# Kernel optimization log

Hardware: AMD Instinct MI355X
Metric: run time of the kernel (lower is better)

## Reference

```python
import math
import jax, jax.numpy as jnp
import numpy as np

NUM_HEADS = 16
LN_EPS = 1e-5


def _ln(x, g, b):
    m = x.mean(-1, keepdims=True)
    v = ((x - m) ** 2).mean(-1, keepdims=True)
    return (x - m) * jax.lax.rsqrt(v + LN_EPS) * g + b


def _rotary_embedding(lat, lon, dim, base=10000.0):
    # spherical-geometry-aware rotary phases; returns sin/cos of shape lat.shape + [dim//2]
    pi = jnp.asarray(math.pi, lat.dtype)
    lon_wrapped = jnp.remainder(lon + pi, 2 * pi) - pi
    lat_c = jnp.clip(lat, -math.pi / 2 + 1e-6, math.pi / 2 - 1e-6)
    scaled_lon = lon_wrapped * jnp.cos(lat_c)
    half = dim // 2
    inv_freq = 1.0 / (base ** (jnp.arange(half, dtype=lat.dtype) / half))
    phase = (lat_c + scaled_lon)[..., None] * inv_freq
    return jnp.sin(phase), jnp.cos(phase)


def _apply_rotary(q, k, sin, cos):
    # q,k: [N, heads, S, hd]; sin/cos: [S, hd//2]
    sin = sin[None, None]
    cos = cos[None, None]
    def rot(x):
        x1 = x[..., 0::2]  # even lanes (torch view(...,hd//2,2).unbind(-1))
        x2 = x[..., 1::2]
        # torch concatenates the two rotated halves (no re-interleave)
        return jnp.concatenate([x1 * cos - x2 * sin, x1 * sin + x2 * cos], axis=-1)
    return rot(q), rot(k)


def _sdpa(q, k, v):
    scale = 1.0 / jnp.sqrt(jnp.asarray(q.shape[-1], q.dtype))
    s = jnp.einsum('nhqd,nhkd->nhqk', q, k) * scale
    return jnp.einsum('nhqk,nhkd->nhqd', jax.nn.softmax(s, axis=-1), v)


def _axial_block(tokens, g, bln, qkv_w, qkv_b, proj_w, proj_b, sincos):
    # tokens: [N, S, D] -> norm -> qkv -> (rope) -> sdpa -> proj -> residual
    N, S, D = tokens.shape
    hd = D // NUM_HEADS
    qkv = _ln(tokens, g, bln) @ qkv_w + qkv_b
    q, k, v = jnp.split(qkv, 3, axis=-1)
    def to_heads(t):
        return t.reshape(N, S, NUM_HEADS, hd).transpose(0, 2, 1, 3)
    q, k, v = to_heads(q), to_heads(k), to_heads(v)
    if sincos is not None:
        q, k = _apply_rotary(q, k, sincos[0], sincos[1])
    o = _sdpa(q, k, v).transpose(0, 2, 1, 3).reshape(N, S, D)
    return tokens + (o @ proj_w + proj_b)


def setup_inputs() -> dict:
    key = jax.random.key(0)
    ks = jax.random.split(key, 8)
    B, L, H, W, D = 1, 13, 48, 96, 512
    x = jax.random.normal(ks[0], (B, L, H, W, D), dtype=jnp.float32)
    lat_grid = jnp.linspace(-math.pi / 2 + 0.01, math.pi / 2 - 0.01, H, dtype=jnp.float32)
    lon_grid = jnp.linspace(-math.pi, math.pi, W, dtype=jnp.float32)  # unused by forward
    s = 0.02
    return {
        'x': x, 'lat_grid': lat_grid, 'lon_grid': lon_grid,
        'lat_qkv_w': s * jax.random.normal(ks[1], (D, 3 * D), jnp.float32),
        'lat_qkv_b': jnp.zeros((3 * D,), jnp.float32),
        'lon_qkv_w': s * jax.random.normal(ks[2], (D, 3 * D), jnp.float32),
        'lon_qkv_b': jnp.zeros((3 * D,), jnp.float32),
        'lev_qkv_w': s * jax.random.normal(ks[3], (D, 3 * D), jnp.float32),
        'lev_qkv_b': jnp.zeros((3 * D,), jnp.float32),
        'proj_w': s * jax.random.normal(ks[4], (D, D), jnp.float32),
        'proj_b': jnp.zeros((D,), jnp.float32),
        'g_lat': jnp.ones((D,), jnp.float32), 'b_lat': jnp.zeros((D,), jnp.float32),
        'g_lon': jnp.ones((D,), jnp.float32), 'b_lon': jnp.zeros((D,), jnp.float32),
        'g_lev': jnp.ones((D,), jnp.float32), 'b_lev': jnp.zeros((D,), jnp.float32),
    }


def reference(x, lat_grid, lon_grid, lat_qkv_w, lat_qkv_b, lon_qkv_w, lon_qkv_b,
              lev_qkv_w, lev_qkv_b, proj_w, proj_b,
              g_lat, b_lat, g_lon, b_lon, g_lev, b_lev):
    B, L, H, W, D = x.shape
    hd = D // NUM_HEADS
    # --- lat axis ---
    lat_tokens = x.transpose(0, 1, 3, 2, 4).reshape(B * L * W, H, D)
    lat_sin, lat_cos = _rotary_embedding(lat_grid, jnp.zeros_like(lat_grid), hd)
    lat_out = _axial_block(lat_tokens, g_lat, b_lat, lat_qkv_w, lat_qkv_b,
                           proj_w, proj_b, (lat_sin, lat_cos))
    lat_out = lat_out.reshape(B, L, W, H, D).transpose(0, 1, 3, 2, 4)
    # --- lon axis ---
    lon_tokens = lat_out.reshape(B * L * H, W, D)
    lon_range = jnp.linspace(-math.pi, math.pi, W, dtype=x.dtype)
    lon_sin, lon_cos = _rotary_embedding(jnp.zeros_like(lon_range), lon_range, hd)
    lon_out = _axial_block(lon_tokens, g_lon, b_lon, lon_qkv_w, lon_qkv_b,
                           proj_w, proj_b, (lon_sin, lon_cos))
    lon_out = lon_out.reshape(B, L, H, W, D)
    # --- level axis (no rotary) ---
    lev_tokens = lon_out.transpose(0, 2, 3, 1, 4).reshape(B * H * W, L, D)
    lev_out = _axial_block(lev_tokens, g_lev, b_lev, lev_qkv_w, lev_qkv_b,
                           proj_w, proj_b, None)
    return lev_out.reshape(B, H, W, L, D).transpose(0, 3, 1, 2, 4)
```

## Files before the change

### kernel.cpp

```cpp
#include <hip/hip_runtime.h>
#include <cstdint>


#define L_DIM 13
#define H_DIM 48
#define W_DIM 96
#define D_DIM 512
#define NH    16
#define MTOK  (L_DIM * H_DIM * W_DIM)
#define N3    (3 * D_DIM)
#define PI_F  3.14159265358979323846f

typedef __bf16 bf16x8 __attribute__((ext_vector_type(8)));
typedef float  f32x4  __attribute__((ext_vector_type(4)));

__device__ __forceinline__ float bf2f(unsigned short u) {
    return __builtin_bit_cast(float, ((unsigned)u) << 16);
}
__device__ __forceinline__ unsigned short f2bf(float f) {
    unsigned u = __builtin_bit_cast(unsigned, f);
    u += 0x7fffu + ((u >> 16) & 1u);
    return (unsigned short)(u >> 16);
}

__global__ __launch_bounds__(256) void copy_f4(const float4* __restrict__ src,
                                               float4* __restrict__ dst, int n4) {
    int i = blockIdx.x * 256 + threadIdx.x;
    if (i < n4) dst[i] = src[i];
}

__global__ __launch_bounds__(256) void transpose_w(const float* __restrict__ w,
                                                   unsigned short* __restrict__ wt, int N) {
    int idx = blockIdx.x * 256 + threadIdx.x;
    if (idx >= 512 * N) return;
    int n = idx >> 9, k = idx & 511;
    wt[idx] = f2bf(w[k * N + n]);
}

__global__ __launch_bounds__(256) void ln_stats(const float* __restrict__ tok,
                                                float* __restrict__ stats) {
    int wv = threadIdx.x >> 6, lane = threadIdx.x & 63;
    int t = blockIdx.x * 4 + wv;
    const float* p = tok + (size_t)t * D_DIM;
    float s = 0.f, s2 = 0.f;
    #pragma unroll
    for (int j = 0; j < 8; ++j) { float v = p[lane + j * 64]; s += v; s2 += v * v; }
    #pragma unroll
    for (int off = 32; off; off >>= 1) {
        s  += __shfl_down(s, off, 64);
        s2 += __shfl_down(s2, off, 64);
    }
    if (lane == 0) {
        float m   = s * (1.f / 512.f);
        float var = s2 * (1.f / 512.f) - m * m;
        stats[t * 2]     = m;
        stats[t * 2 + 1] = rsqrtf(var + 1e-5f);
    }
}

__global__ __launch_bounds__(256) void qkv_gemm(
    const float* __restrict__ tok, const float* __restrict__ stats,
    const float* __restrict__ g, const float* __restrict__ bln,
    const unsigned short* __restrict__ wT, const float* __restrict__ bias,
    unsigned short* __restrict__ out)
{
    __shared__ alignas(16) unsigned short As[128][72];
    __shared__ alignas(16) unsigned short Bs[128][72];
    const int m0 = blockIdx.x * 128, n0 = blockIdx.y * 128;
    const int tid = threadIdx.x, lane = tid & 63, wv = tid >> 6;
    const int wm = (wv >> 1) * 64, wn = (wv & 1) * 64;
    f32x4 acc[4][4] = {};

    for (int k0 = 0; k0 < 512; k0 += 64) {
        #pragma unroll
        for (int i = 0; i < 8; ++i) {
            int c  = tid + i * 256;
            int r  = c >> 4;
            int cc = (c & 15) << 2;
            int gm = m0 + r;
            float4 v = *(const float4*)&tok[(size_t)gm * 512 + k0 + cc];
            float mu = stats[gm * 2], rs = stats[gm * 2 + 1];
            int col = k0 + cc;
            unsigned short* dst = &As[r][cc];
            dst[0] = f2bf((v.x - mu) * rs * g[col]     + bln[col]);
            dst[1] = f2bf((v.y - mu) * rs * g[col + 1] + bln[col + 1]);
            dst[2] = f2bf((v.z - mu) * rs * g[col + 2] + bln[col + 2]);
            dst[3] = f2bf((v.w - mu) * rs * g[col + 3] + bln[col + 3]);
        }
        #pragma unroll
        for (int i = 0; i < 4; ++i) {
            int c = tid + i * 256;
            int r = c >> 3, cc = (c & 7) << 3;
            *(uint4*)&Bs[r][cc] = *(const uint4*)&wT[(size_t)(n0 + r) * 512 + k0 + cc];
        }
        __syncthreads();
        const int ko = (lane >> 4) * 8, lm = lane & 15;
        #pragma unroll
        for (int kk = 0; kk < 64; kk += 32) {
            bf16x8 af[4], bfr[4];
            #pragma unroll
            for (int mi = 0; mi < 4; ++mi) af[mi]  = *(const bf16x8*)&As[wm + mi * 16 + lm][kk + ko];
            #pragma unroll
            for (int ni = 0; ni < 4; ++ni) bfr[ni] = *(const bf16x8*)&Bs[wn + ni * 16 + lm][kk + ko];
            #pragma unroll
            for (int mi = 0; mi < 4; ++mi)
                #pragma unroll
                for (int ni = 0; ni < 4; ++ni)
                    acc[mi][ni] = __builtin_amdgcn_mfma_f32_16x16x32_bf16(af[mi], bfr[ni], acc[mi][ni], 0, 0, 0);
        }
        __syncthreads();
    }
    const int cr = (lane >> 4) * 4, ccol = lane & 15;
    #pragma unroll
    for (int ni = 0; ni < 4; ++ni) {
        int col = n0 + wn + ni * 16 + ccol;
        float bb = bias[col];
        #pragma unroll
        for (int mi = 0; mi < 4; ++mi)
            #pragma unroll
            for (int r = 0; r < 4; ++r) {
                int row = m0 + wm + mi * 16 + cr + r;
                out[(size_t)row * N3 + col] = f2bf(acc[mi][ni][r] + bb);
            }
    }
}

template<int S, int MODE>
__global__ __launch_bounds__(256) void attn_big(
    unsigned short* __restrict__ qkv,
    const float* __restrict__ lat_grid, const float* __restrict__ lon_grid)
{
    constexpr int NQ  = S / 16;
    constexpr int SKP = (S + 31) & ~31;
    constexpr int VST = SKP + 8;
    __shared__ alignas(16) unsigned short qs[S][40];
    __shared__ alignas(16) unsigned short ks[S][40];
    __shared__ alignas(16) unsigned short vT[32][VST];
    __shared__ alignas(16) unsigned short pb[4][16][VST];

    const int n = blockIdx.x, h = blockIdx.y;
    const int tid = threadIdx.x, lane = tid & 63, wv = tid >> 6;
    int base, step;
    if (MODE == 0) { int l = n / 96, w = n - l * 96; base = l * 4608 + w; step = 96; }
    else           { base = n * 96; step = 1; }

    const float SCALE = 0.17677669529663689f;
    for (int idx = tid; idx < S * 16; idx += 256) {
        int s = idx >> 4, i = idx & 15;
        size_t ro = (size_t)(base + s * step) * N3 + h * 32;
        unsigned qp = *(const unsigned*)(qkv + ro + 2 * i);
        unsigned kp = *(const unsigned*)(qkv + ro + 512 + 2 * i);
        unsigned vp = *(const unsigned*)(qkv + ro + 1024 + 2 * i);
        float coord;
        if (MODE == 0) {
            float la = lat_grid[s];
            coord = fminf(fmaxf(la, -PI_F / 2 + 1e-6f), PI_F / 2 - 1e-6f);
        } else {
            float xp = lon_grid[s] + PI_F;
            coord = xp - floorf(xp * (0.5f / PI_F)) * (2.f * PI_F) - PI_F;
        }
        float ph = coord * exp2f(-(float)i * 0.83048202372f);
        float sn = sinf(ph), cs = cosf(ph);
        float q1 = bf2f((unsigned short)qp), q2 = bf2f((unsigned short)(qp >> 16));
        float k1 = bf2f((unsigned short)kp), k2 = bf2f((unsigned short)(kp >> 16));
        qs[s][i]      = f2bf((q1 * cs - q2 * sn) * SCALE);
        qs[s][16 + i] = f2bf((q1 * sn + q2 * cs) * SCALE);
        ks[s][i]      = f2bf(k1 * cs - k2 * sn);
        ks[s][16 + i] = f2bf(k1 * sn + k2 * cs);
        vT[2 * i][s]     = (unsigned short)vp;
        vT[2 * i + 1][s] = (unsigned short)(vp >> 16);
    }
    if (SKP > S) {
        for (int idx = tid; idx < 32 * (SKP - S); idx += 256)
            vT[idx / (SKP - S)][S + idx % (SKP - S)] = 0;
    }
    __syncthreads();

    const int lm = lane & 15, ko = (lane >> 4) * 8, q4 = (lane >> 4) * 4;
    f32x4 zero = {0.f, 0.f, 0.f, 0.f};
    bf16x8 vf[SKP / 32][2];
    #pragma unroll
    for (int u2 = 0; u2 < SKP / 32; ++u2)
        #pragma unroll
        for (int nh2 = 0; nh2 < 2; ++nh2)
            vf[u2][nh2] = *(const bf16x8*)&vT[nh2 * 16 + lm][u2 * 32 + ko];
    if (SKP > S) {
        for (int idx = lane; idx < 16 * (SKP - S); idx += 64)
            pb[wv][idx / (SKP - S)][S + idx % (SKP - S)] = 0;
    }

    for (int t = wv; t < NQ; t += 4) {
        bf16x8 aq = *(const bf16x8*)&qs[t * 16 + lm][ko];
        f32x4 c[NQ];
        #pragma unroll
        for (int u = 0; u < NQ; ++u) {
            bf16x8 bk = *(const bf16x8*)&ks[u * 16 + lm][ko];
            c[u] = __builtin_amdgcn_mfma_f32_16x16x32_bf16(aq, bk, zero, 0, 0, 0);
        }
        float mr[4] = {-1e30f, -1e30f, -1e30f, -1e30f}, sm[4] = {0.f, 0.f, 0.f, 0.f};
        #pragma unroll
        for (int u = 0; u < NQ; ++u)
            #pragma unroll
            for (int r = 0; r < 4; ++r) mr[r] = fmaxf(mr[r], c[u][r]);
        #pragma unroll
        for (int r = 0; r < 4; ++r)
            #pragma unroll
            for (int off = 1; off < 16; off <<= 1)
                mr[r] = fmaxf(mr[r], __shfl_xor(mr[r], off, 64));
        #pragma unroll
        for (int u = 0; u < NQ; ++u)
            #pragma unroll
            for (int r = 0; r < 4; ++r) {
                float e = __expf(c[u][r] - mr[r]);
                c[u][r] = e; sm[r] += e;
            }
        #pragma unroll
        for (int r = 0; r < 4; ++r) {
            #pragma unroll
            for (int off = 1; off < 16; off <<= 1)
                sm[r] += __shfl_xor(sm[r], off, 64);
            sm[r] = 1.f / sm[r];
        }
        #pragma unroll
        for (int u = 0; u < NQ; ++u)
            #pragma unroll
            for (int r = 0; r < 4; ++r)
                pb[wv][q4 + r][u * 16 + lm] = f2bf(c[u][r] * sm[r]);
        __builtin_amdgcn_wave_barrier();
        f32x4 o0 = zero, o1 = zero;
        #pragma unroll
        for (int u2 = 0; u2 < SKP / 32; ++u2) {
            bf16x8 ap = *(const bf16x8*)&pb[wv][lm][u2 * 32 + ko];
            o0 = __builtin_amdgcn_mfma_f32_16x16x32_bf16(ap, vf[u2][0], o0, 0, 0, 0);
            o1 = __builtin_amdgcn_mfma_f32_16x16x32_bf16(ap, vf[u2][1], o1, 0, 0, 0);
        }
        __builtin_amdgcn_wave_barrier();
        #pragma unroll
        for (int r = 0; r < 4; ++r) {
            int row = t * 16 + q4 + r;
            size_t ro = (size_t)(base + row * step) * N3 + h * 32;
            qkv[ro + lm]      = f2bf(o0[r]);
            qkv[ro + 16 + lm] = f2bf(o1[r]);
        }
    }
}

__global__ __launch_bounds__(256) void attn_small(unsigned short* __restrict__ qkv)
{
    __shared__ alignas(16) unsigned short qs[4][16][40];
    __shared__ alignas(16) unsigned short ks[4][16][40];
    __shared__ alignas(16) unsigned short vT[4][32][40];
    __shared__ alignas(16) unsigned short pb[4][16][40];
    const int tid = threadIdx.x, lane = tid & 63, wv = tid >> 6;
    const int pair = blockIdx.x * 4 + wv;
    const int n = pair >> 4, h = pair & 15;
    const int base = n, step = 4608;

    for (int idx = lane; idx < 13 * 16; idx += 64) {
        int s = idx >> 4, i = idx & 15;
        size_t ro = (size_t)(base + s * step) * N3 + h * 32;
        *(unsigned*)&qs[wv][s][2 * i] = *(const unsigned*)(qkv + ro + 2 * i);
        *(unsigned*)&ks[wv][s][2 * i] = *(const unsigned*)(qkv + ro + 512 + 2 * i);
        unsigned vp = *(const unsigned*)(qkv + ro + 1024 + 2 * i);
        vT[wv][2 * i][s]     = (unsigned short)vp;
        vT[wv][2 * i + 1][s] = (unsigned short)(vp >> 16);
    }
    for (int idx = lane; idx < 32 * 19; idx += 64) {
        int d = idx / 19, k = 13 + idx % 19;
        vT[wv][d][k] = 0;
    }
    for (int idx = lane; idx < 16 * 16; idx += 64)
        pb[wv][idx >> 4][16 + (idx & 15)] = 0;
    __syncthreads();

    const int lm = lane & 15, ko = (lane >> 4) * 8, q4 = (lane >> 4) * 4;
    f32x4 zero = {0.f, 0.f, 0.f, 0.f};
    bf16x8 aq = *(const bf16x8*)&qs[wv][lm][ko];
    bf16x8 bk = *(const bf16x8*)&ks[wv][lm][ko];
    f32x4 c = __builtin_amdgcn_mfma_f32_16x16x32_bf16(aq, bk, zero, 0, 0, 0);
    const float SCALE = 0.17677669529663689f;
    float cf[4], mr[4], sm[4];
    bool colok = (lm < 13);
    #pragma unroll
    for (int r = 0; r < 4; ++r) {
        cf[r] = colok ? c[r] * SCALE : -1e30f;
        mr[r] = cf[r];
    }
    #pragma unroll
    for (int r = 0; r < 4; ++r)
        #pragma unroll
        for (int off = 1; off < 16; off <<= 1)
            mr[r] = fmaxf(mr[r], __shfl_xor(mr[r], off, 64));
    #pragma unroll
    for (int r = 0; r < 4; ++r) { cf[r] = __expf(cf[r] - mr[r]); sm[r] = cf[r]; }
    #pragma unroll
    for (int r = 0; r < 4; ++r) {
        #pragma unroll
        for (int off = 1; off < 16; off <<= 1)
            sm[r] += __shfl_xor(sm[r], off, 64);
        sm[r] = 1.f / sm[r];
    }
    #pragma unroll
    for (int r = 0; r < 4; ++r)
        pb[wv][q4 + r][lm] = f2bf(cf[r] * sm[r]);
    __builtin_amdgcn_wave_barrier();
    bf16x8 ap  = *(const bf16x8*)&pb[wv][lm][ko];
    bf16x8 vf0 = *(const bf16x8*)&vT[wv][lm][ko];
    bf16x8 vf1 = *(const bf16x8*)&vT[wv][16 + lm][ko];
    f32x4 o0 = __builtin_amdgcn_mfma_f32_16x16x32_bf16(ap, vf0, zero, 0, 0, 0);
    f32x4 o1 = __builtin_amdgcn_mfma_f32_16x16x32_bf16(ap, vf1, zero, 0, 0, 0);
    #pragma unroll
    for (int r = 0; r < 4; ++r) {
        int row = q4 + r;
        if (row < 13) {
            size_t ro = (size_t)(base + row * step) * N3 + h * 32;
            qkv[ro + lm]      = f2bf(o0[r]);
            qkv[ro + 16 + lm] = f2bf(o1[r]);
        }
    }
}

__global__ __launch_bounds__(256) void proj_gemm(
    const unsigned short* __restrict__ attn,
    const unsigned short* __restrict__ pT, const float* __restrict__ pb,
    float* __restrict__ tok)
{
    __shared__ alignas(16) unsigned short As[128][72];
    __shared__ alignas(16) unsigned short Bs[128][72];
    const int m0 = blockIdx.x * 128, n0 = blockIdx.y * 128;
    const int tid = threadIdx.x, lane = tid & 63, wv = tid >> 6;
    const int wm = (wv >> 1) * 64, wn = (wv & 1) * 64;
    f32x4 acc[4][4] = {};

    for (int k0 = 0; k0 < 512; k0 += 64) {
        #pragma unroll
        for (int i = 0; i < 4; ++i) {
            int c = tid + i * 256;
            int r = c >> 3, cc = (c & 7) << 3;
            *(uint4*)&As[r][cc] = *(const uint4*)&attn[(size_t)(m0 + r) * N3 + k0 + cc];
        }
        #pragma unroll
        for (int i = 0; i < 4; ++i) {
            int c = tid + i * 256;
            int r = c >> 3, cc = (c & 7) << 3;
            *(uint4*)&Bs[r][cc] = *(const uint4*)&pT[(size_t)(n0 + r) * 512 + k0 + cc];
        }
        __syncthreads();
        const int ko = (lane >> 4) * 8, lm = lane & 15;
        #pragma unroll
        for (int kk = 0; kk < 64; kk += 32) {
            bf16x8 af[4], bfr[4];
            #pragma unroll
            for (int mi = 0; mi < 4; ++mi) af[mi]  = *(const bf16x8*)&As[wm + mi * 16 + lm][kk + ko];
            #pragma unroll
            for (int ni = 0; ni < 4; ++ni) bfr[ni] = *(const bf16x8*)&Bs[wn + ni * 16 + lm][kk + ko];
            #pragma unroll
            for (int mi = 0; mi < 4; ++mi)
                #pragma unroll
                for (int ni = 0; ni < 4; ++ni)
                    acc[mi][ni] = __builtin_amdgcn_mfma_f32_16x16x32_bf16(af[mi], bfr[ni], acc[mi][ni], 0, 0, 0);
        }
        __syncthreads();
    }
    const int cr = (lane >> 4) * 4, ccol = lane & 15;
    #pragma unroll
    for (int ni = 0; ni < 4; ++ni) {
        int col = n0 + wn + ni * 16 + ccol;
        float bb = pb[col];
        #pragma unroll
        for (int mi = 0; mi < 4; ++mi)
            #pragma unroll
            for (int r = 0; r < 4; ++r) {
                int row = m0 + wm + mi * 16 + cr + r;
                size_t a = (size_t)row * 512 + col;
                tok[a] = tok[a] + acc[mi][ni][r] + bb;
            }
    }
}

extern "C" void kernel_launch(void* const* d_in, const int* in_sizes, int n_in,
                              void* d_out, int out_size, void* d_ws, size_t ws_size,
                              hipStream_t stream) {
    const float* x        = (const float*)d_in[0];
    const float* lat_grid = (const float*)d_in[1];
    const float* lon_grid = (const float*)d_in[2];
    const float* qkv_w[3] = {(const float*)d_in[3], (const float*)d_in[5], (const float*)d_in[7]};
    const float* qkv_b[3] = {(const float*)d_in[4], (const float*)d_in[6], (const float*)d_in[8]};
    const float* proj_w   = (const float*)d_in[9];
    const float* proj_b   = (const float*)d_in[10];
    const float* g[3]     = {(const float*)d_in[11], (const float*)d_in[13], (const float*)d_in[15]};
    const float* bln[3]   = {(const float*)d_in[12], (const float*)d_in[14], (const float*)d_in[16]};
    float* tok = (float*)d_out;

    unsigned short* wT0 = (unsigned short*)d_ws;
    unsigned short* wT1 = wT0 + 1536 * 512;
    unsigned short* wT2 = wT1 + 1536 * 512;
    unsigned short* pT  = wT2 + 1536 * 512;
    float*          stats = (float*)(pT + 512 * 512);
    unsigned short* qkv = (unsigned short*)(stats + 2 * MTOK);
    unsigned short* wT[3] = {wT0, wT1, wT2};

    copy_f4<<<(MTOK * 512 / 4) / 256, 256, 0, stream>>>((const float4*)x, (float4*)tok, MTOK * 512 / 4);
    transpose_w<<<(512 * 1536) / 256, 256, 0, stream>>>(qkv_w[0], wT0, 1536);
    transpose_w<<<(512 * 1536) / 256, 256, 0, stream>>>(qkv_w[1], wT1, 1536);
    transpose_w<<<(512 * 1536) / 256, 256, 0, stream>>>(qkv_w[2], wT2, 1536);
    transpose_w<<<(512 * 512) / 256, 256, 0, stream>>>(proj_w, pT, 512);

    for (int b = 0; b < 3; ++b) {
        ln_stats<<<MTOK / 4, 256, 0, stream>>>(tok, stats);
        qkv_gemm<<<dim3(MTOK / 128, N3 / 128), 256, 0, stream>>>(
            tok, stats, g[b], bln[b], wT[b], qkv_b[b], qkv);
        if (b == 0)
            attn_big<48, 0><<<dim3(L_DIM * W_DIM, NH), 256, 0, stream>>>(qkv, lat_grid, lon_grid);
        else if (b == 1)
            attn_big<96, 1><<<dim3(L_DIM * H_DIM, NH), 256, 0, stream>>>(qkv, lat_grid, lon_grid);
        else
            attn_small<<<(H_DIM * W_DIM * NH) / 4, 256, 0, stream>>>(qkv);
        proj_gemm<<<dim3(MTOK / 128, 512 / 128), 256, 0, stream>>>(qkv, pT, proj_b, tok);
    }
}
```

Before: 1.516 ms.

## Precompute LayerNorm to bf16 and stream GEMM tiles via global_load_lds

LayerNorm is now applied once per token in a separate kernel that writes a bf16 buffer. Before, the QKV GEMM recomputed the normalisation and fp32-to-bf16 conversion for every N tile. Both GEMMs now load A and B tiles straight into LDS with 16-byte global_load_lds, and the launch grid is swapped so N tiles are the fastest-varying index, which should improve L2 reuse of the A rows. The LDS padding is dropped to fit the direct-load layout, which may add bank conflicts on the fragment reads. The change also costs an extra bf16 activation buffer write and read.

Measured after the change: 1.385 ms. 8.7% less time.

```diff
diff --git a/kernel.cpp b/kernel.cpp
--- a/kernel.cpp
+++ b/kernel.cpp
@@ -22,6 +22,11 @@
     u += 0x7fffu + ((u >> 16) & 1u);
     return (unsigned short)(u >> 16);
 }
+__device__ __forceinline__ void gload16(unsigned short* lds, const unsigned short* g) {
+    __builtin_amdgcn_global_load_lds(
+        (const __attribute__((address_space(1))) unsigned int*)g,
+        (__attribute__((address_space(3))) unsigned int*)lds, 16, 0, 0);
+}
 
 __global__ __launch_bounds__(256) void copy_f4(const float4* __restrict__ src,
                                                float4* __restrict__ dst, int n4) {
@@ -37,61 +42,62 @@
     wt[idx] = f2bf(w[k * N + n]);
 }
 
-__global__ __launch_bounds__(256) void ln_stats(const float* __restrict__ tok,
-                                                float* __restrict__ stats) {
+__global__ __launch_bounds__(256) void ln_apply(
+    const float* __restrict__ tok, const float* __restrict__ g,
+    const float* __restrict__ bln, unsigned short* __restrict__ out)
+{
     int wv = threadIdx.x >> 6, lane = threadIdx.x & 63;
     int t = blockIdx.x * 4 + wv;
-    const float* p = tok + (size_t)t * D_DIM;
-    float s = 0.f, s2 = 0.f;
-    #pragma unroll
-    for (int j = 0; j < 8; ++j) { float v = p[lane + j * 64]; s += v; s2 += v * v; }
-    #pragma unroll
-    for (int off = 32; off; off >>= 1) {
-        s  += __shfl_down(s, off, 64);
-        s2 += __shfl_down(s2, off, 64);
-    }
-    if (lane == 0) {
-        float m   = s * (1.f / 512.f);
-        float var = s2 * (1.f / 512.f) - m * m;
-        stats[t * 2]     = m;
-        stats[t * 2 + 1] = rsqrtf(var + 1e-5f);
-    }
+    const float* p = tok + (size_t)t * 512 + lane * 8;
+    float4 a = *(const float4*)p, b = *(const float4*)(p + 4);
+    float s  = a.x + a.y + a.z + a.w + b.x + b.y + b.z + b.w;
+    float s2 = a.x*a.x + a.y*a.y + a.z*a.z + a.w*a.w + b.x*b.x + b.y*b.y + b.z*b.z + b.w*b.w;
+    #pragma unroll
+    for (int off = 1; off < 64; off <<= 1) {
+        s  += __shfl_xor(s, off, 64);
+        s2 += __shfl_xor(s2, off, 64);
+    }
+    float mu = s * (1.f / 512.f);
+    float rs = rsqrtf(s2 * (1.f / 512.f) - mu * mu + 1e-5f);
+    float4 g0 = *(const float4*)(g + lane * 8),  g1 = *(const float4*)(g + lane * 8 + 4);
+    float4 b0 = *(const float4*)(bln + lane * 8), b1 = *(const float4*)(bln + lane * 8 + 4);
+    unsigned short o[8];
+    o[0] = f2bf((a.x - mu) * rs * g0.x + b0.x);
+    o[1] = f2bf((a.y - mu) * rs * g0.y + b0.y);
+    o[2] = f2bf((a.z - mu) * rs * g0.z + b0.z);
+    o[3] = f2bf((a.w - mu) * rs * g0.w + b0.w);
+    o[4] = f2bf((b.x - mu) * rs * g1.x + b1.x);
+    o[5] = f2bf((b.y - mu) * rs * g1.y + b1.y);
+    o[6] = f2bf((b.z - mu) * rs * g1.z + b1.z);
+    o[7] = f2bf((b.w - mu) * rs * g1.w + b1.w);
+    uint4 r;
+    r.x = (unsigned)o[0] | ((unsigned)o[1] << 16);
+    r.y = (unsigned)o[2] | ((unsigned)o[3] << 16);
+    r.z = (unsigned)o[4] | ((unsigned)o[5] << 16);
+    r.w = (unsigned)o[6] | ((unsigned)o[7] << 16);
+    *(uint4*)&out[(size_t)t * 512 + lane * 8] = r;
 }
 
 __global__ __launch_bounds__(256) void qkv_gemm(
-    const float* __restrict__ tok, const float* __restrict__ stats,
-    const float* __restrict__ g, const float* __restrict__ bln,
+    const unsigned short* __restrict__ lnb,
     const unsigned short* __restrict__ wT, const float* __restrict__ bias,
     unsigned short* __restrict__ out)
 {
-    __shared__ alignas(16) unsigned short As[128][72];
-    __shared__ alignas(16) unsigned short Bs[128][72];
-    const int m0 = blockIdx.x * 128, n0 = blockIdx.y * 128;
+    __shared__ alignas(16) unsigned short As[128][64];
+    __shared__ alignas(16) unsigned short Bs[128][64];
+    const int n0 = blockIdx.x * 128, m0 = blockIdx.y * 128;
     const int tid = threadIdx.x, lane = tid & 63, wv = tid >> 6;
     const int wm = (wv >> 1) * 64, wn = (wv & 1) * 64;
+    const int srow = lane >> 3, scol = (lane & 7) * 8;
     f32x4 acc[4][4] = {};
 
     for (int k0 = 0; k0 < 512; k0 += 64) {
         #pragma unroll
-        for (int i = 0; i < 8; ++i) {
-            int c  = tid + i * 256;
-            int r  = c >> 4;
-            int cc = (c & 15) << 2;
-            int gm = m0 + r;
-            float4 v = *(const float4*)&tok[(size_t)gm * 512 + k0 + cc];
-            float mu = stats[gm * 2], rs = stats[gm * 2 + 1];
-            int col = k0 + cc;
-            unsigned short* dst = &As[r][cc];
-            dst[0] = f2bf((v.x - mu) * rs * g[col]     + bln[col]);
-            dst[1] = f2bf((v.y - mu) * rs * g[col + 1] + bln[col + 1]);
-            dst[2] = f2bf((v.z - mu) * rs * g[col + 2] + bln[col + 2]);
-            dst[3] = f2bf((v.w - mu) * rs * g[col + 3] + bln[col + 3]);
-        }
-        #pragma unroll
         for (int i = 0; i < 4; ++i) {
-            int c = tid + i * 256;
-            int r = c >> 3, cc = (c & 7) << 3;
-            *(uint4*)&Bs[r][cc] = *(const uint4*)&wT[(size_t)(n0 + r) * 512 + k0 + cc];
+            int c = i * 4 + wv;
+            int r = c * 8 + srow;
+            gload16(&As[c * 8][0], &lnb[(size_t)(m0 + r) * 512 + k0 + scol]);
+            gload16(&Bs[c * 8][0], &wT [(size_t)(n0 + r) * 512 + k0 + scol]);
         }
         __syncthreads();
         const int ko = (lane >> 4) * 8, lm = lane & 15;
@@ -325,25 +331,21 @@
     const unsigned short* __restrict__ pT, const float* __restrict__ pb,
     float* __restrict__ tok)
 {
-    __shared__ alignas(16) unsigned short As[128][72];
-    __shared__ alignas(16) unsigned short Bs[128][72];
-    const int m0 = blockIdx.x * 128, n0 = blockIdx.y * 128;
+    __shared__ alignas(16) unsigned short As[128][64];
+    __shared__ alignas(16) unsigned short Bs[128][64];
+    const int n0 = blockIdx.x * 128, m0 = blockIdx.y * 128;
     const int tid = threadIdx.x, lane = tid & 63, wv = tid >> 6;
     const int wm = (wv >> 1) * 64, wn = (wv & 1) * 64;
+    const int srow = lane >> 3, scol = (lane & 7) * 8;
     f32x4 acc[4][4] = {};
 
     for (int k0 = 0; k0 < 512; k0 += 64) {
         #pragma unroll
         for (int i = 0; i < 4; ++i) {
-            int c = tid + i * 256;
-            int r = c >> 3, cc = (c & 7) << 3;
-            *(uint4*)&As[r][cc] = *(const uint4*)&attn[(size_t)(m0 + r) * N3 + k0 + cc];
-        }
-        #pragma unroll
-        for (int i = 0; i < 4; ++i) {
-            int c = tid + i * 256;
-            int r = c >> 3, cc = (c & 7) << 3;
-            *(uint4*)&Bs[r][cc] = *(const uint4*)&pT[(size_t)(n0 + r) * 512 + k0 + cc];
+            int c = i * 4 + wv;
+            int r = c * 8 + srow;
+            gload16(&As[c * 8][0], &attn[(size_t)(m0 + r) * N3 + k0 + scol]);
+            gload16(&Bs[c * 8][0], &pT [(size_t)(n0 + r) * 512 + k0 + scol]);
         }
         __syncthreads();
         const int ko = (lane >> 4) * 8, lm = lane & 15;
@@ -396,8 +398,8 @@
     unsigned short* wT1 = wT0 + 1536 * 512;
     unsigned short* wT2 = wT1 + 1536 * 512;
     unsigned short* pT  = wT2 + 1536 * 512;
-    float*          stats = (float*)(pT + 512 * 512);
-    unsigned short* qkv = (unsigned short*)(stats + 2 * MTOK);
+    unsigned short* lnb = pT + 512 * 512;
+    unsigned short* qkv = lnb + (size_t)MTOK * 512;
     unsigned short* wT[3] = {wT0, wT1, wT2};
 
     copy_f4<<<(MTOK * 512 / 4) / 256, 256, 0, stream>>>((const float4*)x, (float4*)tok, MTOK * 512 / 4);
@@ -407,15 +409,14 @@
     transpose_w<<<(512 * 512) / 256, 256, 0, stream>>>(proj_w, pT, 512);
 
     for (int b = 0; b < 3; ++b) {
-        ln_stats<<<MTOK / 4, 256, 0, stream>>>(tok, stats);
-        qkv_gemm<<<dim3(MTOK / 128, N3 / 128), 256, 0, stream>>>(
-            tok, stats, g[b], bln[b], wT[b], qkv_b[b], qkv);
+        ln_apply<<<MTOK / 4, 256, 0, stream>>>(tok, g[b], bln[b], lnb);
+        qkv_gemm<<<dim3(N3 / 128, MTOK / 128), 256, 0, stream>>>(lnb, wT[b], qkv_b[b], qkv);
         if (b == 0)
             attn_big<48, 0><<<dim3(L_DIM * W_DIM, NH), 256, 0, stream>>>(qkv, lat_grid, lon_grid);
         else if (b == 1)
             attn_big<96, 1><<<dim3(L_DIM * H_DIM, NH), 256, 0, stream>>>(qkv, lat_grid, lon_grid);
         else
             attn_small<<<(H_DIM * W_DIM * NH) / 4, 256, 0, stream>>>(qkv);
-        proj_gemm<<<dim3(MTOK / 128, 512 / 128), 256, 0, stream>>>(qkv, pT, proj_b, tok);
-    }
-}
+        proj_gemm<<<dim3(512 / 128, MTOK / 128), 256, 0, stream>>>(qkv, pT, proj_b, tok);
+    }
+}
```
